# Performance work log

Measured on AMD Instinct MI355X. Metric: run time of the kernel, lower is better.

## Reference

```python
import jax, jax.numpy as jnp
import numpy as np

N = 384      # max_nodes
H = 256      # layers[0] == layers[1] == layers[2]
Z = 128      # dim_z
ED = 128     # edge_dim
AH = ED // 2 # attention hidden

# complete directed graph: combinations (i<j) then reversed pairs
_i, _j = np.triu_indices(N, k=1)
_SRC = jnp.asarray(np.concatenate([_i, _j]), dtype=jnp.int32)  # edge_index[0]
_DST = jnp.asarray(np.concatenate([_j, _i]), dtype=jnp.int32)  # edge_index[1]


def setup_inputs() -> dict:
    key = jax.random.key(0)
    ks = jax.random.split(key, 16)
    def p(k, shape, fan_in):
        return jax.random.normal(k, shape, dtype=jnp.float32) * (1.0 / np.sqrt(fan_in))
    return {
        "z": jax.random.normal(ks[0], (1, Z), dtype=jnp.float32),
        # GRU (torch layout: W_ih [3H, Z], W_hh [3H, H]; gate order r, z, n)
        "gru_Wih": p(ks[1], (3 * H, Z), Z),
        "gru_Whh": p(ks[2], (3 * H, H), H),
        "gru_bih": jnp.zeros((3 * H,), jnp.float32),
        "gru_bhh": jnp.zeros((3 * H,), jnp.float32),
        # edge_generator MLP: 2H -> 4H -> ED
        "eg_W1": p(ks[3], (2 * H, 4 * H), 2 * H), "eg_b1": jnp.zeros((4 * H,), jnp.float32),
        "eg_W2": p(ks[4], (4 * H, ED), 4 * H),   "eg_b2": jnp.zeros((ED,), jnp.float32),
        # attention MLPs: (ED+H) -> ED//2 -> 1
        "att0_W1": p(ks[5], (ED + H, AH), ED + H), "att0_b1": jnp.zeros((AH,), jnp.float32),
        "att0_W2": p(ks[6], (AH, 1), AH),           "att0_b2": jnp.zeros((1,), jnp.float32),
        "att1_W1": p(ks[7], (ED + H, AH), ED + H), "att1_b1": jnp.zeros((AH,), jnp.float32),
        "att1_W2": p(ks[8], (AH, 1), AH),           "att1_b2": jnp.zeros((1,), jnp.float32),
        # EdgeConv output linears: H -> H
        "conv0_W": p(ks[9], (H, H), H),  "conv0_b": jnp.zeros((H,), jnp.float32),
        "conv1_W": p(ks[10], (H, H), H), "conv1_b": jnp.zeros((H,), jnp.float32),
    }


def _forward(z, gru_Wih, gru_Whh, gru_bih, gru_bhh,
             eg_W1, eg_b1, eg_W2, eg_b2,
             att0_W1, att0_b1, att0_W2, att0_b2,
             att1_W1, att1_b1, att1_W2, att1_b2,
             conv0_W, conv0_b, conv1_W, conv1_b):
    # --- GRU node generation: input is the same latent z at every step ---
    gi = z[0] @ gru_Wih.T + gru_bih            # [3H], constant per step
    gir, giz, gin = jnp.split(gi, 3)
    def step(h, _):
        gh = h @ gru_Whh.T + gru_bhh
        ghr, ghz, ghn = jnp.split(gh, 3)
        r = jax.nn.sigmoid(gir + ghr)
        u = jax.nn.sigmoid(giz + ghz)
        n = jnp.tanh(gin + r * ghn)
        h2 = (1.0 - u) * n + u * h
        return h2, h2
    _, nodes = jax.lax.scan(step, jnp.zeros((H,), z.dtype), None, length=N)  # [N, H]

    # --- edge features over the complete directed graph ---
    pairs = jnp.concatenate([nodes[_SRC], nodes[_DST]], axis=-1)            # [E, 2H]
    edges = jax.nn.relu(pairs @ eg_W1 + eg_b1) @ eg_W2 + eg_b2              # [E, ED]

    # --- EdgeConv: gather src, attention MLP gate, scatter-sum, linear ---
    def conv(x, aW1, ab1, aW2, ab2, W, b):
        xs = x[_SRC]                                                        # [E, H]
        a_in = jnp.concatenate([edges, xs], axis=-1)                        # [E, ED+H]
        att = jax.nn.sigmoid(jax.nn.relu(a_in @ aW1 + ab1) @ aW2 + ab2)     # [E, 1]
        agg = jax.ops.segment_sum(att * xs, _DST, num_segments=N)           # [N, H]
        return agg @ W + b

    x = jax.nn.relu(conv(nodes, att0_W1, att0_b1, att0_W2, att0_b2, conv0_W, conv0_b))
    x = conv(x, att1_W1, att1_b1, att1_W2, att1_b2, conv1_W, conv1_b)
    return jnp.sum(x, axis=0)                                               # [H]


def reference(z, gru_Wih, gru_Whh, gru_bih, gru_bhh,
              eg_W1, eg_b1, eg_W2, eg_b2,
              att0_W1, att0_b1, att0_W2, att0_b2,
              att1_W1, att1_b1, att1_W2, att1_b2,
              conv0_W, conv0_b, conv1_W, conv1_b):
    return _forward(z, gru_Wih, gru_Whh, gru_bih, gru_bhh,
                    eg_W1, eg_b1, eg_W2, eg_b2,
                    att0_W1, att0_b1, att0_W2, att0_b2,
                    att1_W1, att1_b1, att1_W2, att1_b2,
                    conv0_W, conv0_b, conv1_W, conv1_b)
```

## Files before the change

kernel.cpp:

```cpp
#include <hip/hip_runtime.h>
#include <hip/hip_fp16.h>
#include <cstdint>

#define DEV static __device__ __forceinline__

typedef _Float16 h2v __attribute__((ext_vector_type(2)));
typedef _Float16 half8 __attribute__((ext_vector_type(8)));
typedef float float4v __attribute__((ext_vector_type(4)));

union U32H2 { uint32_t u; _Float16 f[2]; };

DEV uint32_t pack_f2(float a, float b) {
    auto p = __builtin_amdgcn_cvt_pkrtz(a, b);
    return __builtin_bit_cast(uint32_t, p);
}

DEV half8 bc8(uint4 v) { return __builtin_bit_cast(half8, v); }

DEV void gl_lds16(const void* gsrc, void* ldst) {
    __builtin_amdgcn_global_load_lds(
        (const __attribute__((address_space(1))) uint32_t*)gsrc,
        (__attribute__((address_space(3))) uint32_t*)ldst, 16, 0, 0);
}

DEV float pick4(float4v lo, float4v hi, int bsel, int r) {
    float v0 = bsel ? hi[0] : lo[0];
    float v1 = bsel ? hi[1] : lo[1];
    float v2 = bsel ? hi[2] : lo[2];
    float v3 = bsel ? hi[3] : lo[3];
    float x01 = (r & 1) ? v1 : v0;
    float x23 = (r & 1) ? v3 : v2;
    return (r & 2) ? x23 : x01;
}

static const size_t OFF_W16T  = 0;
static const size_t OFF_GI    = 98304;
static const size_t OFF_CC    = 99072;
static const size_t OFF_BF    = 99200;
static const size_t OFF_NODES = 164736;
static const size_t OFF_PF    = 263040;
static const size_t OFF_QF    = 459648;
static const size_t OFF_R0    = 656256;
static const size_t OFF_R1    = 680832;
static const size_t OFF_TT    = 705408;
static const size_t OFF_ATT0  = 10142592;
static const size_t OFF_ATT1  = 10290048;
static const size_t OFF_X0    = 10535808;
static const size_t OFF_CS    = 10634112;
static const size_t WS_TOTAL  = 10634816;

__global__ void k_prep_wl(const float* __restrict__ Whh, uint32_t* __restrict__ WL,
                          const float* __restrict__ z, const float* __restrict__ Wih,
                          const float* __restrict__ bih, const float* __restrict__ bhh,
                          float* __restrict__ gs) {
    int bb = blockIdx.x, tid = threadIdx.x;
    if (bb < 48) {
        int c = bb;
        int rt = c >> 3, kt = c & 7;
        int lane = tid & 63, wv = tid >> 6;
        int row = (rt >> 1) * 256 + wv * 32 + ((rt & 1) << 4) + (lane & 15);
        int k0 = kt*32 + (lane >> 4)*8;
        const float* src = Whh + row*256 + k0;
        uint4 o;
        o.x = pack_f2(src[0], src[1]);
        o.y = pack_f2(src[2], src[3]);
        o.z = pack_f2(src[4], src[5]);
        o.w = pack_f2(src[6], src[7]);
        ((uint4*)WL)[c*512 + tid] = o;
    } else {
        int o = (bb - 48) * 512 + tid;
        if (o < 768) {
            float acc = bih[o];
            if (o < 512) acc += bhh[o];
            for (int i = 0; i < 128; ++i) acc += Wih[o*128 + i] * z[i];
            gs[o] = acc;
        }
    }
}

__global__ void __launch_bounds__(512, 2)
k_gru_bf(const float* __restrict__ gs, const float* __restrict__ bhh,
         const uint32_t* __restrict__ WL, float* __restrict__ nodes,
         const float* __restrict__ egW2, const float* __restrict__ egb2,
         const float* __restrict__ a0W1, const float* __restrict__ a1W1,
         uint32_t* __restrict__ BF, float* __restrict__ cc) {
    int bb = blockIdx.x, tid = threadIdx.x;
    if (bb == 0) {
        __shared__ __align__(16) _Float16 hh16[512];
        int lane = tid & 63, wv = tid >> 6;
        int kq = lane >> 4, c = lane & 15;
        const float L2E = 1.44269504088896f;
        int r = c & 3, bsel = (c >> 2) & 1;
        int gidx = wv*32 + kq*4 + r + bsel*16;
        bool active = (c < 8);

        uint4 w[48];
        const uint4* wl4 = (const uint4*)WL;
        #pragma unroll
        for (int q = 0; q < 48; ++q) w[q] = wl4[q*512 + tid];
        #pragma unroll
        for (int q = 0; q < 48; ++q)
            asm volatile("" : "+a"(w[q].x), "+a"(w[q].y), "+a"(w[q].z), "+a"(w[q].w));

        float pr = -L2E * gs[gidx];
        float pz = -L2E * gs[256 + gidx];
        float pn = -2.f * L2E * gs[512 + gidx];
        float bn_l = bhh[512 + gidx];

        float h = 0.f;
        if (tid < 256) ((uint32_t*)hh16)[tid] = 0u;
        __syncthreads();

        const float4v z4 = {0.f, 0.f, 0.f, 0.f};
        int par = 0;
        for (int t = 0; t < 384; ++t) {
            const _Float16* hb = hh16 + par*256 + kq*8;
            uint4 b[8];
            #pragma unroll
            for (int kt = 0; kt < 8; ++kt) b[kt] = *(const uint4*)(hb + kt*32);

            float4v d0, d1, d2, d3, d4, d5;
            d0 = __builtin_amdgcn_mfma_f32_16x16x32_f16(bc8(w[0]),  bc8(b[0]), z4, 0, 0, 0);
            d1 = __builtin_amdgcn_mfma_f32_16x16x32_f16(bc8(w[8]),  bc8(b[0]), z4, 0, 0, 0);
            #pragma unroll
            for (int kt = 1; kt < 8; ++kt) {
                d0 = __builtin_amdgcn_mfma_f32_16x16x32_f16(bc8(w[kt]),   bc8(b[kt]), d0, 0, 0, 0);
                d1 = __builtin_amdgcn_mfma_f32_16x16x32_f16(bc8(w[8+kt]), bc8(b[kt]), d1, 0, 0, 0);
            }
            float ghr = pick4(d0, d1, bsel, r);
            float er = __builtin_amdgcn_exp2f(__builtin_fmaf(ghr, -L2E, pr));
            float rg = __builtin_amdgcn_rcpf(1.f + er);

            d2 = __builtin_amdgcn_mfma_f32_16x16x32_f16(bc8(w[16]), bc8(b[0]), z4, 0, 0, 0);
            d3 = __builtin_amdgcn_mfma_f32_16x16x32_f16(bc8(w[24]), bc8(b[0]), z4, 0, 0, 0);
            d4 = __builtin_amdgcn_mfma_f32_16x16x32_f16(bc8(w[32]), bc8(b[0]), z4, 0, 0, 0);
            d5 = __builtin_amdgcn_mfma_f32_16x16x32_f16(bc8(w[40]), bc8(b[0]), z4, 0, 0, 0);
            #pragma unroll
            for (int kt = 1; kt < 8; ++kt) {
                d2 = __builtin_amdgcn_mfma_f32_16x16x32_f16(bc8(w[16+kt]), bc8(b[kt]), d2, 0, 0, 0);
                d3 = __builtin_amdgcn_mfma_f32_16x16x32_f16(bc8(w[24+kt]), bc8(b[kt]), d3, 0, 0, 0);
                d4 = __builtin_amdgcn_mfma_f32_16x16x32_f16(bc8(w[32+kt]), bc8(b[kt]), d4, 0, 0, 0);
                d5 = __builtin_amdgcn_mfma_f32_16x16x32_f16(bc8(w[40+kt]), bc8(b[kt]), d5, 0, 0, 0);
            }

            float ghz = pick4(d2, d3, bsel, r);
            float ghn = pick4(d4, d5, bsel, r);
            float eu = __builtin_amdgcn_exp2f(__builtin_fmaf(ghz, -L2E, pz));
            float u  = __builtin_amdgcn_rcpf(1.f + eu);
            float tm = ghn + bn_l;
            float q  = __builtin_fmaf(rg * tm, -2.f * L2E, pn);
            float e2 = __builtin_amdgcn_exp2f(q);
            float nn = __builtin_fmaf(2.f, __builtin_amdgcn_rcpf(1.f + e2), -1.f);
            h = nn + u * (h - nn);

            if (active) {
                hh16[(par ^ 1)*256 + gidx] = (_Float16)h;
                nodes[t*256 + gidx] = h;
            }
            asm volatile("s_waitcnt lgkmcnt(0)" ::: "memory");
            __builtin_amdgcn_sched_barrier(0);
            __builtin_amdgcn_s_barrier();
            __builtin_amdgcn_sched_barrier(0);
            par ^= 1;
        }
    } else if (bb < 129) {
        int idx = (bb - 1) * 512 + tid;
        int k2 = idx >> 7, n = idx & 127;
        const float* A = (n < 64) ? (a0W1 + n) : (a1W1 + (n - 64));
        const float* w0 = egW2 + (2*k2) * 128;
        float a = 0.f, b = 0.f;
        for (int i = 0; i < 128; ++i) {
            float av = A[i*64];
            a += w0[i] * av;
            b += w0[128 + i] * av;
        }
        int kk = k2 >> 4, jgrp = (k2 >> 2) & 3, sub = k2 & 3;
        int lane = jgrp*16 + (n & 15), t = n >> 4;
        BF[((kk*8 + t)*64 + lane)*4 + sub] = pack_f2(a, b);
    } else {
        if (tid < 128) {
            const float* A = (tid < 64) ? a0W1 : a1W1;
            int j = tid & 63;
            float acc = 0.f;
            for (int i = 0; i < 128; ++i) acc += egb2[i] * A[i*64 + j];
            cc[tid] = acc;
        }
    }
}

__global__ void k_pq(const float* __restrict__ nodes, const float* __restrict__ eg_W1,
                     const float* __restrict__ eg_b1, const float* __restrict__ a0W1,
                     const float* __restrict__ a0b1, const float* __restrict__ cc,
                     uint32_t* __restrict__ PF, uint32_t* __restrict__ QF,
                     float* __restrict__ R0) {
    int tid = threadIdx.x;
    int s0 = blockIdx.x * 4;
    __shared__ float ns[4][256];
    #pragma unroll
    for (int q = 0; q < 4; ++q) ns[q][tid] = nodes[(s0+q)*256 + tid];
    __syncthreads();

    int k0 = tid * 4;
    float acc[4][4];
    #pragma unroll
    for (int q = 0; q < 4; ++q) { acc[q][0]=0;acc[q][1]=0;acc[q][2]=0;acc[q][3]=0; }
    for (int i = 0; i < 256; ++i) {
        float4 wv = *(const float4*)&eg_W1[i*1024 + k0];
        #pragma unroll
        for (int q = 0; q < 4; ++q) {
            float nv = ns[q][i];
            acc[q][0] += nv*wv.x; acc[q][1] += nv*wv.y;
            acc[q][2] += nv*wv.z; acc[q][3] += nv*wv.w;
        }
    }
    float4 bv = *(const float4*)&eg_b1[k0];
    {
        int kk = k0 >> 5;
        int lgrp = ((k0 >> 3) & 3) * 16;
        int sub = (k0 & 7) >> 1;
        #pragma unroll
        for (int q = 0; q < 4; ++q) {
            int s = s0 + q, g = s >> 4, srow = s & 15;
            uint2 pw;
            pw.x = pack_f2(acc[q][0] + bv.x, acc[q][1] + bv.y);
            pw.y = pack_f2(acc[q][2] + bv.z, acc[q][3] + bv.w);
            *(uint2*)(PF + (((g*32 + kk)*64 + lgrp + srow) << 2) + sub) = pw;
        }
    }

    #pragma unroll
    for (int q = 0; q < 4; ++q) { acc[q][0]=0;acc[q][1]=0;acc[q][2]=0;acc[q][3]=0; }
    for (int i = 0; i < 256; ++i) {
        float4 wv = *(const float4*)&eg_W1[(256+i)*1024 + k0];
        #pragma unroll
        for (int q = 0; q < 4; ++q) {
            float nv = ns[q][i];
            acc[q][0] += nv*wv.x; acc[q][1] += nv*wv.y;
            acc[q][2] += nv*wv.z; acc[q][3] += nv*wv.w;
        }
    }
    #pragma unroll
    for (int q = 0; q < 4; ++q) {
        uint2 pw;
        pw.x = pack_f2(acc[q][0], acc[q][1]);
        pw.y = pack_f2(acc[q][2], acc[q][3]);
        ((uint2*)QF)[(s0+q)*256 + tid] = pw;
    }

    int srow = tid >> 6, j = tid & 63;
    float racc = a0b1[j] + cc[j];
    for (int i = 0; i < 256; ++i) racc += ns[srow][i] * a0W1[(128+i)*64 + j];
    R0[(s0+srow)*64 + j] = racc;
}

__global__ void __launch_bounds__(512, 4)
k_phaseA(const uint32_t* __restrict__ PF, const uint32_t* __restrict__ QF,
         const uint32_t* __restrict__ BF, const float* __restrict__ R0,
         const float* __restrict__ a0W2, const float* __restrict__ a0b2,
         uint32_t* __restrict__ TT, float* __restrict__ ATT0) {
    __shared__ __align__(16) char smem[69632];
    uint4* Qs4 = (uint4*)smem;
    char* bufbase = smem + 32768;
    int tid = threadIdx.x;
    int lane = tid & 63, wv = tid >> 6;
    int g = blockIdx.x, dt = blockIdx.y, d0 = dt * 16;

    {
        const char* src = (const char*)(QF + (size_t)d0 * 512);
        for (int off = tid*16; off < 32768; off += 8192)
            gl_lds16(src + off, (char*)Qs4 + off);
    }
    {
        const char* psrc = (const char*)(PF + (size_t)g * 8192);
        if (tid < 128) gl_lds16(psrc + tid*16, bufbase + tid*16);
        const char* bsrc = (const char*)BF;
        #pragma unroll
        for (int i = 0; i < 2; ++i)
            gl_lds16(bsrc + tid*16 + i*8192, bufbase + 2048 + tid*16 + i*8192);
    }
    asm volatile("s_waitcnt vmcnt(0)" ::: "memory");
    __builtin_amdgcn_sched_barrier(0);
    __builtin_amdgcn_s_barrier();
    __builtin_amdgcn_sched_barrier(0);

    float4v acc[2][8];
    #pragma unroll
    for (int t = 0; t < 2; ++t)
        #pragma unroll
        for (int n = 0; n < 8; ++n) acc[t][n] = 0.f;

    for (int hc = 0; hc < 16; ++hc) {
        char* cur = bufbase + (hc & 1) * 18432;
        char* nxt = bufbase + ((hc + 1) & 1) * 18432;
        if (hc < 15) {
            const char* psrc = (const char*)(PF + ((size_t)g*32 + (size_t)(hc+1)*2) * 256);
            if (tid < 128) gl_lds16(psrc + tid*16, nxt + tid*16);
            const char* bsrc = (const char*)(BF + (size_t)(hc+1) * 4096);
            #pragma unroll
            for (int i = 0; i < 2; ++i)
                gl_lds16(bsrc + tid*16 + i*8192, nxt + 2048 + tid*16 + i*8192);
        }
        uint4* Ph = (uint4*)cur;
        uint4* Bh = (uint4*)(cur + 2048);
        #pragma unroll
        for (int kkl = 0; kkl < 2; ++kkl) {
            int kkg = hc*2 + kkl;
            half8 b[8];
            #pragma unroll
            for (int n = 0; n < 8; ++n) b[n] = bc8(Bh[(kkl*8 + n)*64 + lane]);
            half8 p8 = bc8(Ph[kkl*64 + lane]);
            #pragma unroll
            for (int t = 0; t < 2; ++t) {
                half8 q8 = bc8(Qs4[(wv*2 + t)*128 + kkg*4 + (lane >> 4)]);
                half8 x = p8 + q8;
                half8 zz = 0;
                x = __builtin_elementwise_max(x, zz);
                #pragma unroll
                for (int n = 0; n < 8; ++n)
                    acc[t][n] = __builtin_amdgcn_mfma_f32_16x16x32_f16(x, b[n], acc[t][n], 0, 0, 0);
            }
        }
        asm volatile("s_waitcnt vmcnt(0)" ::: "memory");
        __builtin_amdgcn_sched_barrier(0);
        __builtin_amdgcn_s_barrier();
        __builtin_amdgcn_sched_barrier(0);
    }

    __syncthreads();
    float* R0s = (float*)smem;
    float* w2s = (float*)(smem + 4096);
    for (int i = tid; i < 1024; i += 512)
        R0s[i] = R0[(size_t)(g*16 + (i >> 6))*64 + (i & 63)];
    if (tid < 64) w2s[tid] = a0W2[tid];
    float b2v = a0b2[0];

    _Float16* epi = (_Float16*)(smem + 32768);
    int cn = lane & 15, rhi = (lane >> 4) * 4;
    for (int half = 0; half < 2; ++half) {
        __syncthreads();
        #pragma unroll
        for (int t = 0; t < 2; ++t) {
            int dl = wv*2 + t;
            #pragma unroll
            for (int n = 0; n < 4; ++n) {
                int j = n*16 + cn;
                float4v v = acc[t][half*4 + n];
                #pragma unroll
                for (int r = 0; r < 4; ++r)
                    epi[((rhi + r)*16 + dl)*64 + j] = (_Float16)v[r];
            }
        }
        __syncthreads();
        if (half == 1) {
            int p = tid >> 1, sub = tid & 1;
            int srow = p >> 4, dl = p & 15;
            const uint4* src = (const uint4*)(epi + (size_t)p*64);
            uint4* dst = (uint4*)(TT + ((size_t)((g*16 + srow)*384 + d0 + dl))*32);
            #pragma unroll
            for (int q = 0; q < 4; ++q) dst[sub*4 + q] = src[sub*4 + q];
        }
        if (half == 0 && tid < 256) {
            int sl = tid >> 4, dl = tid & 15;
            const _Float16* tp = epi + (size_t)(sl*16 + dl)*64;
            const float* rp = R0s + sl*64;
            float logit = b2v;
            #pragma unroll
            for (int j = 0; j < 64; ++j)
                logit += fmaxf((float)tp[j] + rp[j], 0.f) * w2s[j];
            float a = 1.f / (1.f + __expf(-logit));
            int s = g*16 + sl, d = d0 + dl;
            ATT0[(size_t)s*384 + d] = (s == d) ? 0.f : a;
        }
    }
}

__global__ void k_att(const uint32_t* __restrict__ TT, const float* __restrict__ R,
                      const float* __restrict__ w2, const float* __restrict__ b2,
                      float* __restrict__ ATT, float* __restrict__ CS) {
    int tid = threadIdx.x;
    int p = blockIdx.x * 256 + tid;
    int s = p / 384, d = p - s * 384;
    int sa = (blockIdx.x * 256) / 384;
    __shared__ float w2s[64];
    __shared__ float rs[2][64];
    if (tid < 64) w2s[tid] = w2[tid];
    else if (tid < 128) rs[0][tid - 64] = R[sa*64 + (tid - 64)];
    else if (tid < 192) {
        int sb = sa + 1;
        rs[1][tid - 128] = (sb < 384) ? R[sb*64 + (tid - 128)] : 0.f;
    }
    __syncthreads();
    const uint4* tp = (const uint4*)(TT + (size_t)p*32);
    const float* rp = (s == sa) ? rs[0] : rs[1];
    float logit = b2[0];
    #pragma unroll
    for (int m = 0; m < 8; ++m) {
        uint4 tv = tp[m];
        uint32_t us[4] = {tv.x, tv.y, tv.z, tv.w};
        #pragma unroll
        for (int q = 0; q < 4; ++q) {
            U32H2 c; c.u = us[q];
            int j = m*8 + q*2;
            float h0 = fmaxf((float)c.f[0] + rp[j],   0.f);
            float h1 = fmaxf((float)c.f[1] + rp[j+1], 0.f);
            logit += h0*w2s[j] + h1*w2s[j+1];
        }
    }
    float a = 1.f / (1.f + __expf(-logit));
    float a_eff = (s == d) ? 0.f : a;
    ATT[p] = a_eff;

    float va = (s == sa) ? a_eff : 0.f;
    float vb = (s != sa) ? a_eff : 0.f;
    #pragma unroll
    for (int o = 32; o > 0; o >>= 1) {
        va += __shfl_down(va, o, 64);
        vb += __shfl_down(vb, o, 64);
    }
    if ((tid & 63) == 0) {
        atomicAdd(&CS[sa], va);
        int sb = sa + 1;
        if (sb < 384) atomicAdd(&CS[sb], vb);
    }
}

__global__ void __launch_bounds__(256)
k_aggx0(const float* __restrict__ ATT, const float* __restrict__ X,
        const float* __restrict__ W, const float* __restrict__ b,
        const float* __restrict__ a1W1, const float* __restrict__ a1b1,
        const float* __restrict__ cc,
        float* __restrict__ X0, float* __restrict__ R1, float* __restrict__ CS) {
    int d = blockIdx.x, tid = threadIdx.x;
    if (d == 0) {
        for (int s = tid; s < 384; s += 256) CS[s] = 0.f;
    }
    __shared__ float att_col[384];
    __shared__ float ag[256];
    __shared__ float xs[256];
    for (int s = tid; s < 384; s += 256) att_col[s] = ATT[(size_t)s*384 + d];
    __syncthreads();
    float acc = 0.f;
    #pragma unroll 4
    for (int s = 0; s < 384; ++s)
        acc += att_col[s] * X[(size_t)s*256 + tid];
    ag[tid] = acc;
    __syncthreads();
    float x0 = b[tid];
    for (int i = 0; i < 256; ++i) x0 += ag[i] * W[i*256 + tid];
    x0 = fmaxf(x0, 0.f);
    X0[(size_t)d*256 + tid] = x0;
    xs[tid] = x0;
    __syncthreads();
    if (tid < 64) {
        float r = a1b1[tid] + cc[64 + tid];
        for (int i = 0; i < 256; ++i) r += xs[i] * a1W1[(128+i)*64 + tid];
        R1[(size_t)d*64 + tid] = r;
    }
}

__global__ void k_vout(const float* __restrict__ CS, const float* __restrict__ X0,
                       const float* __restrict__ W, const float* __restrict__ b,
                       float* __restrict__ out) {
    int tid = threadIdx.x;
    __shared__ float cs[384];
    __shared__ float vs[256];
    for (int q = tid; q < 384; q += 256) cs[q] = CS[q];
    __syncthreads();
    float acc = 0.f;
    for (int s = 0; s < 384; s += 4) {
        acc += cs[s]*X0[s*256 + tid] + cs[s+1]*X0[(s+1)*256 + tid]
             + cs[s+2]*X0[(s+2)*256 + tid] + cs[s+3]*X0[(s+3)*256 + tid];
    }
    vs[tid] = acc;
    __syncthreads();
    float o = 384.f * b[tid];
    for (int i = 0; i < 256; ++i) o += vs[i] * W[i*256 + tid];
    out[tid] = o;
}

extern "C" void kernel_launch(void* const* d_in, const int* in_sizes, int n_in,
                              void* d_out, int out_size, void* d_ws, size_t ws_size,
                              hipStream_t stream) {
    if (ws_size < WS_TOTAL * sizeof(uint32_t)) return;

    const float* z    = (const float*)d_in[0];
    const float* Wih  = (const float*)d_in[1];
    const float* Whh  = (const float*)d_in[2];
    const float* bih  = (const float*)d_in[3];
    const float* bhh  = (const float*)d_in[4];
    const float* egW1 = (const float*)d_in[5];
    const float* egb1 = (const float*)d_in[6];
    const float* egW2 = (const float*)d_in[7];
    const float* egb2 = (const float*)d_in[8];
    const float* a0W1 = (const float*)d_in[9];
    const float* a0b1 = (const float*)d_in[10];
    const float* a0W2 = (const float*)d_in[11];
    const float* a0b2 = (const float*)d_in[12];
    const float* a1W1 = (const float*)d_in[13];
    const float* a1b1 = (const float*)d_in[14];
    const float* a1W2 = (const float*)d_in[15];
    const float* a1b2 = (const float*)d_in[16];
    const float* c0W  = (const float*)d_in[17];
    const float* c0b  = (const float*)d_in[18];
    const float* c1W  = (const float*)d_in[19];
    const float* c1b  = (const float*)d_in[20];

    uint32_t* ws   = (uint32_t*)d_ws;
    uint32_t* WL   = ws + OFF_W16T;
    float*    gs   = (float*)(ws + OFF_GI);
    float*    cc   = (float*)(ws + OFF_CC);
    uint32_t* BF   = ws + OFF_BF;
    float*    nodes= (float*)(ws + OFF_NODES);
    uint32_t* PF   = ws + OFF_PF;
    uint32_t* QF   = ws + OFF_QF;
    float*    R0   = (float*)(ws + OFF_R0);
    float*    R1   = (float*)(ws + OFF_R1);
    uint32_t* TT   = ws + OFF_TT;
    float*    ATT0 = (float*)(ws + OFF_ATT0);
    float*    ATT1 = (float*)(ws + OFF_ATT1);
    float*    X0   = (float*)(ws + OFF_X0);
    float*    CS   = (float*)(ws + OFF_CS);
    float*    out  = (float*)d_out;

    hipLaunchKernelGGL(k_prep_wl, dim3(50),     dim3(512), 0, stream, Whh, WL, z, Wih, bih, bhh, gs);
    hipLaunchKernelGGL(k_gru_bf,  dim3(130),    dim3(512), 0, stream, gs, bhh, WL, nodes,
                       egW2, egb2, a0W1, a1W1, BF, cc);
    hipLaunchKernelGGL(k_pq,      dim3(96),     dim3(256), 0, stream, nodes, egW1, egb1, a0W1, a0b1, cc, PF, QF, R0);
    hipLaunchKernelGGL(k_phaseA,  dim3(24, 24), dim3(512), 0, stream, PF, QF, BF, R0, a0W2, a0b2, TT, ATT0);
    hipLaunchKernelGGL(k_aggx0,   dim3(384),    dim3(256), 0, stream, ATT0, nodes, c0W, c0b, a1W1, a1b1, cc, X0, R1, CS);
    hipLaunchKernelGGL(k_att,     dim3(576),    dim3(256), 0, stream, TT, R1, a1W2, a1b2, ATT1, CS);
    hipLaunchKernelGGL(k_vout,    dim3(1),      dim3(256), 0, stream, CS, X0, c1W, c1b, out);
}
```

Baseline: 664.1 us.

## Split GRU recurrence across kernels to overlap node projection with tail steps

The 384-step GRU is split into two launches: the first runs steps 0-287, and the second runs steps 288-383 in block 0 while 36 other blocks compute the edge-MLP/attention projections (P, Q, R0) for the first 288 nodes. A small tail kernel then handles the remaining 96 nodes. The projection kernel is also widened to 512 threads and 8 nodes per block, with P and Q handled by separate thread halves. The unused ATT1 store in k_att is removed. The aim is to hide projection work behind the serial recurrence, at the cost of an extra launch and reloading the GRU weights into registers a second time.

After: 650.4 us, median of 2. 2.1% less time.

```diff
diff --git a/kernel.cpp b/kernel.cpp
--- a/kernel.cpp
+++ b/kernel.cpp
@@ -78,91 +78,158 @@
     }
 }
 
+DEV void gru_run(const float* __restrict__ gs, const float* __restrict__ bhh,
+                 const uint32_t* __restrict__ WL, float* __restrict__ nodes,
+                 _Float16* hh16, int tid, int t0, int t1) {
+    int lane = tid & 63, wv = tid >> 6;
+    int kq = lane >> 4, c = lane & 15;
+    const float L2E = 1.44269504088896f;
+    int r = c & 3, bsel = (c >> 2) & 1;
+    int gidx = wv*32 + kq*4 + r + bsel*16;
+    bool active = (c < 8);
+
+    uint4 w[48];
+    const uint4* wl4 = (const uint4*)WL;
+    #pragma unroll
+    for (int q = 0; q < 48; ++q) w[q] = wl4[q*512 + tid];
+    #pragma unroll
+    for (int q = 0; q < 48; ++q)
+        asm volatile("" : "+a"(w[q].x), "+a"(w[q].y), "+a"(w[q].z), "+a"(w[q].w));
+
+    float pr = -L2E * gs[gidx];
+    float pz = -L2E * gs[256 + gidx];
+    float pn = -2.f * L2E * gs[512 + gidx];
+    float bn_l = bhh[512 + gidx];
+
+    float h;
+    if (t0 == 0) {
+        h = 0.f;
+        if (tid < 256) ((uint32_t*)hh16)[tid] = 0u;
+    } else {
+        h = nodes[(size_t)(t0-1)*256 + gidx];
+        if (tid < 256) hh16[tid] = (_Float16)nodes[(size_t)(t0-1)*256 + tid];
+    }
+    __syncthreads();
+
+    const float4v z4 = {0.f, 0.f, 0.f, 0.f};
+    int par = 0;
+    for (int t = t0; t < t1; ++t) {
+        const _Float16* hb = hh16 + par*256 + kq*8;
+        uint4 b[8];
+        #pragma unroll
+        for (int kt = 0; kt < 8; ++kt) b[kt] = *(const uint4*)(hb + kt*32);
+
+        float4v d0, d1, d2, d3, d4, d5;
+        d0 = __builtin_amdgcn_mfma_f32_16x16x32_f16(bc8(w[0]),  bc8(b[0]), z4, 0, 0, 0);
+        d1 = __builtin_amdgcn_mfma_f32_16x16x32_f16(bc8(w[8]),  bc8(b[0]), z4, 0, 0, 0);
+        #pragma unroll
+        for (int kt = 1; kt < 8; ++kt) {
+            d0 = __builtin_amdgcn_mfma_f32_16x16x32_f16(bc8(w[kt]),   bc8(b[kt]), d0, 0, 0, 0);
+            d1 = __builtin_amdgcn_mfma_f32_16x16x32_f16(bc8(w[8+kt]), bc8(b[kt]), d1, 0, 0, 0);
+        }
+        float ghr = pick4(d0, d1, bsel, r);
+        float er = __builtin_amdgcn_exp2f(__builtin_fmaf(ghr, -L2E, pr));
+        float rg = __builtin_amdgcn_rcpf(1.f + er);
+
+        d2 = __builtin_amdgcn_mfma_f32_16x16x32_f16(bc8(w[16]), bc8(b[0]), z4, 0, 0, 0);
+        d3 = __builtin_amdgcn_mfma_f32_16x16x32_f16(bc8(w[24]), bc8(b[0]), z4, 0, 0, 0);
+        d4 = __builtin_amdgcn_mfma_f32_16x16x32_f16(bc8(w[32]), bc8(b[0]), z4, 0, 0, 0);
+        d5 = __builtin_amdgcn_mfma_f32_16x16x32_f16(bc8(w[40]), bc8(b[0]), z4, 0, 0, 0);
+        #pragma unroll
+        for (int kt = 1; kt < 8; ++kt) {
+            d2 = __builtin_amdgcn_mfma_f32_16x16x32_f16(bc8(w[16+kt]), bc8(b[kt]), d2, 0, 0, 0);
+            d3 = __builtin_amdgcn_mfma_f32_16x16x32_f16(bc8(w[24+kt]), bc8(b[kt]), d3, 0, 0, 0);
+            d4 = __builtin_amdgcn_mfma_f32_16x16x32_f16(bc8(w[32+kt]), bc8(b[kt]), d4, 0, 0, 0);
+            d5 = __builtin_amdgcn_mfma_f32_16x16x32_f16(bc8(w[40+kt]), bc8(b[kt]), d5, 0, 0, 0);
+        }
+
+        float ghz = pick4(d2, d3, bsel, r);
+        float ghn = pick4(d4, d5, bsel, r);
+        float eu = __builtin_amdgcn_exp2f(__builtin_fmaf(ghz, -L2E, pz));
+        float u  = __builtin_amdgcn_rcpf(1.f + eu);
+        float tm = ghn + bn_l;
+        float q  = __builtin_fmaf(rg * tm, -2.f * L2E, pn);
+        float e2 = __builtin_amdgcn_exp2f(q);
+        float nn = __builtin_fmaf(2.f, __builtin_amdgcn_rcpf(1.f + e2), -1.f);
+        h = nn + u * (h - nn);
+
+        if (active) {
+            hh16[(par ^ 1)*256 + gidx] = (_Float16)h;
+            nodes[(size_t)t*256 + gidx] = h;
+        }
+        asm volatile("s_waitcnt lgkmcnt(0)" ::: "memory");
+        __builtin_amdgcn_sched_barrier(0);
+        __builtin_amdgcn_s_barrier();
+        __builtin_amdgcn_sched_barrier(0);
+        par ^= 1;
+    }
+}
+
+DEV void pq8_body(const float* __restrict__ nodes, const float* __restrict__ egW1,
+                  const float* __restrict__ egb1, const float* __restrict__ a0W1,
+                  const float* __restrict__ a0b1, const float* __restrict__ cc,
+                  uint32_t* __restrict__ PF, uint32_t* __restrict__ QF,
+                  float* __restrict__ R0, int s0, int tid, float* ns) {
+    for (int i = tid; i < 2048; i += 512)
+        ns[i] = nodes[(size_t)s0*256 + i];
+    __syncthreads();
+
+    int tp = tid & 255;
+    int k0 = tp * 4;
+    bool isQ = tid >= 256;
+    float acc[8][4];
+    #pragma unroll
+    for (int q = 0; q < 8; ++q) { acc[q][0]=0;acc[q][1]=0;acc[q][2]=0;acc[q][3]=0; }
+    const float* Wbase = egW1 + (isQ ? (size_t)256*1024 : 0) + k0;
+    for (int i = 0; i < 256; ++i) {
+        float4 wv = *(const float4*)&Wbase[(size_t)i*1024];
+        #pragma unroll
+        for (int q = 0; q < 8; ++q) {
+            float nv = ns[q*256 + i];
+            acc[q][0] += nv*wv.x; acc[q][1] += nv*wv.y;
+            acc[q][2] += nv*wv.z; acc[q][3] += nv*wv.w;
+        }
+    }
+    if (!isQ) {
+        float4 bv = *(const float4*)&egb1[k0];
+        int kk = k0 >> 5;
+        int lgrp = ((k0 >> 3) & 3) * 16;
+        int sub = (k0 & 7) >> 1;
+        #pragma unroll
+        for (int q = 0; q < 8; ++q) {
+            int s = s0 + q, g = s >> 4, srow = s & 15;
+            uint2 pw;
+            pw.x = pack_f2(acc[q][0] + bv.x, acc[q][1] + bv.y);
+            pw.y = pack_f2(acc[q][2] + bv.z, acc[q][3] + bv.w);
+            *(uint2*)(PF + (((g*32 + kk)*64 + lgrp + srow) << 2) + sub) = pw;
+        }
+    } else {
+        #pragma unroll
+        for (int q = 0; q < 8; ++q) {
+            uint2 pw;
+            pw.x = pack_f2(acc[q][0], acc[q][1]);
+            pw.y = pack_f2(acc[q][2], acc[q][3]);
+            ((uint2*)QF)[(size_t)(s0+q)*256 + tp] = pw;
+        }
+    }
+    {
+        int srow = tid >> 6, j = tid & 63;
+        float racc = a0b1[j] + cc[j];
+        for (int i = 0; i < 256; ++i) racc += ns[srow*256 + i] * a0W1[(128+i)*64 + j];
+        R0[(size_t)(s0+srow)*64 + j] = racc;
+    }
+}
+
 __global__ void __launch_bounds__(512, 2)
-k_gru_bf(const float* __restrict__ gs, const float* __restrict__ bhh,
-         const uint32_t* __restrict__ WL, float* __restrict__ nodes,
-         const float* __restrict__ egW2, const float* __restrict__ egb2,
-         const float* __restrict__ a0W1, const float* __restrict__ a1W1,
-         uint32_t* __restrict__ BF, float* __restrict__ cc) {
+k_gruA_bf(const float* __restrict__ gs, const float* __restrict__ bhh,
+          const uint32_t* __restrict__ WL, float* __restrict__ nodes,
+          const float* __restrict__ egW2, const float* __restrict__ egb2,
+          const float* __restrict__ a0W1, const float* __restrict__ a1W1,
+          uint32_t* __restrict__ BF, float* __restrict__ cc) {
     int bb = blockIdx.x, tid = threadIdx.x;
     if (bb == 0) {
         __shared__ __align__(16) _Float16 hh16[512];
-        int lane = tid & 63, wv = tid >> 6;
-        int kq = lane >> 4, c = lane & 15;
-        const float L2E = 1.44269504088896f;
-        int r = c & 3, bsel = (c >> 2) & 1;
-        int gidx = wv*32 + kq*4 + r + bsel*16;
-        bool active = (c < 8);
-
-        uint4 w[48];
-        const uint4* wl4 = (const uint4*)WL;
-        #pragma unroll
-        for (int q = 0; q < 48; ++q) w[q] = wl4[q*512 + tid];
-        #pragma unroll
-        for (int q = 0; q < 48; ++q)
-            asm volatile("" : "+a"(w[q].x), "+a"(w[q].y), "+a"(w[q].z), "+a"(w[q].w));
-
-        float pr = -L2E * gs[gidx];
-        float pz = -L2E * gs[256 + gidx];
-        float pn = -2.f * L2E * gs[512 + gidx];
-        float bn_l = bhh[512 + gidx];
-
-        float h = 0.f;
-        if (tid < 256) ((uint32_t*)hh16)[tid] = 0u;
-        __syncthreads();
-
-        const float4v z4 = {0.f, 0.f, 0.f, 0.f};
-        int par = 0;
-        for (int t = 0; t < 384; ++t) {
-            const _Float16* hb = hh16 + par*256 + kq*8;
-            uint4 b[8];
-            #pragma unroll
-            for (int kt = 0; kt < 8; ++kt) b[kt] = *(const uint4*)(hb + kt*32);
-
-            float4v d0, d1, d2, d3, d4, d5;
-            d0 = __builtin_amdgcn_mfma_f32_16x16x32_f16(bc8(w[0]),  bc8(b[0]), z4, 0, 0, 0);
-            d1 = __builtin_amdgcn_mfma_f32_16x16x32_f16(bc8(w[8]),  bc8(b[0]), z4, 0, 0, 0);
-            #pragma unroll
-            for (int kt = 1; kt < 8; ++kt) {
-                d0 = __builtin_amdgcn_mfma_f32_16x16x32_f16(bc8(w[kt]),   bc8(b[kt]), d0, 0, 0, 0);
-                d1 = __builtin_amdgcn_mfma_f32_16x16x32_f16(bc8(w[8+kt]), bc8(b[kt]), d1, 0, 0, 0);
-            }
-            float ghr = pick4(d0, d1, bsel, r);
-            float er = __builtin_amdgcn_exp2f(__builtin_fmaf(ghr, -L2E, pr));
-            float rg = __builtin_amdgcn_rcpf(1.f + er);
-
-            d2 = __builtin_amdgcn_mfma_f32_16x16x32_f16(bc8(w[16]), bc8(b[0]), z4, 0, 0, 0);
-            d3 = __builtin_amdgcn_mfma_f32_16x16x32_f16(bc8(w[24]), bc8(b[0]), z4, 0, 0, 0);
-            d4 = __builtin_amdgcn_mfma_f32_16x16x32_f16(bc8(w[32]), bc8(b[0]), z4, 0, 0, 0);
-            d5 = __builtin_amdgcn_mfma_f32_16x16x32_f16(bc8(w[40]), bc8(b[0]), z4, 0, 0, 0);
-            #pragma unroll
-            for (int kt = 1; kt < 8; ++kt) {
-                d2 = __builtin_amdgcn_mfma_f32_16x16x32_f16(bc8(w[16+kt]), bc8(b[kt]), d2, 0, 0, 0);
-                d3 = __builtin_amdgcn_mfma_f32_16x16x32_f16(bc8(w[24+kt]), bc8(b[kt]), d3, 0, 0, 0);
-                d4 = __builtin_amdgcn_mfma_f32_16x16x32_f16(bc8(w[32+kt]), bc8(b[kt]), d4, 0, 0, 0);
-                d5 = __builtin_amdgcn_mfma_f32_16x16x32_f16(bc8(w[40+kt]), bc8(b[kt]), d5, 0, 0, 0);
-            }
-
-            float ghz = pick4(d2, d3, bsel, r);
-            float ghn = pick4(d4, d5, bsel, r);
-            float eu = __builtin_amdgcn_exp2f(__builtin_fmaf(ghz, -L2E, pz));
-            float u  = __builtin_amdgcn_rcpf(1.f + eu);
-            float tm = ghn + bn_l;
-            float q  = __builtin_fmaf(rg * tm, -2.f * L2E, pn);
-            float e2 = __builtin_amdgcn_exp2f(q);
-            float nn = __builtin_fmaf(2.f, __builtin_amdgcn_rcpf(1.f + e2), -1.f);
-            h = nn + u * (h - nn);
-
-            if (active) {
-                hh16[(par ^ 1)*256 + gidx] = (_Float16)h;
-                nodes[t*256 + gidx] = h;
-            }
-            asm volatile("s_waitcnt lgkmcnt(0)" ::: "memory");
-            __builtin_amdgcn_sched_barrier(0);
-            __builtin_amdgcn_s_barrier();
-            __builtin_amdgcn_sched_barrier(0);
-            par ^= 1;
-        }
+        gru_run(gs, bhh, WL, nodes, hh16, tid, 0, 288);
     } else if (bb < 129) {
         int idx = (bb - 1) * 512 + tid;
         int k2 = idx >> 7, n = idx & 127;
@@ -188,69 +255,32 @@
     }
 }
 
-__global__ void k_pq(const float* __restrict__ nodes, const float* __restrict__ eg_W1,
-                     const float* __restrict__ eg_b1, const float* __restrict__ a0W1,
-                     const float* __restrict__ a0b1, const float* __restrict__ cc,
-                     uint32_t* __restrict__ PF, uint32_t* __restrict__ QF,
-                     float* __restrict__ R0) {
-    int tid = threadIdx.x;
-    int s0 = blockIdx.x * 4;
-    __shared__ float ns[4][256];
-    #pragma unroll
-    for (int q = 0; q < 4; ++q) ns[q][tid] = nodes[(s0+q)*256 + tid];
-    __syncthreads();
-
-    int k0 = tid * 4;
-    float acc[4][4];
-    #pragma unroll
-    for (int q = 0; q < 4; ++q) { acc[q][0]=0;acc[q][1]=0;acc[q][2]=0;acc[q][3]=0; }
-    for (int i = 0; i < 256; ++i) {
-        float4 wv = *(const float4*)&eg_W1[i*1024 + k0];
-        #pragma unroll
-        for (int q = 0; q < 4; ++q) {
-            float nv = ns[q][i];
-            acc[q][0] += nv*wv.x; acc[q][1] += nv*wv.y;
-            acc[q][2] += nv*wv.z; acc[q][3] += nv*wv.w;
-        }
-    }
-    float4 bv = *(const float4*)&eg_b1[k0];
-    {
-        int kk = k0 >> 5;
-        int lgrp = ((k0 >> 3) & 3) * 16;
-        int sub = (k0 & 7) >> 1;
-        #pragma unroll
-        for (int q = 0; q < 4; ++q) {
-            int s = s0 + q, g = s >> 4, srow = s & 15;
-            uint2 pw;
-            pw.x = pack_f2(acc[q][0] + bv.x, acc[q][1] + bv.y);
-            pw.y = pack_f2(acc[q][2] + bv.z, acc[q][3] + bv.w);
-            *(uint2*)(PF + (((g*32 + kk)*64 + lgrp + srow) << 2) + sub) = pw;
-        }
-    }
-
-    #pragma unroll
-    for (int q = 0; q < 4; ++q) { acc[q][0]=0;acc[q][1]=0;acc[q][2]=0;acc[q][3]=0; }
-    for (int i = 0; i < 256; ++i) {
-        float4 wv = *(const float4*)&eg_W1[(256+i)*1024 + k0];
-        #pragma unroll
-        for (int q = 0; q < 4; ++q) {
-            float nv = ns[q][i];
-            acc[q][0] += nv*wv.x; acc[q][1] += nv*wv.y;
-            acc[q][2] += nv*wv.z; acc[q][3] += nv*wv.w;
-        }
-    }
-    #pragma unroll
-    for (int q = 0; q < 4; ++q) {
-        uint2 pw;
-        pw.x = pack_f2(acc[q][0], acc[q][1]);
-        pw.y = pack_f2(acc[q][2], acc[q][3]);
-        ((uint2*)QF)[(s0+q)*256 + tid] = pw;
-    }
-
-    int srow = tid >> 6, j = tid & 63;
-    float racc = a0b1[j] + cc[j];
-    for (int i = 0; i < 256; ++i) racc += ns[srow][i] * a0W1[(128+i)*64 + j];
-    R0[(s0+srow)*64 + j] = racc;
+__global__ void __launch_bounds__(512, 2)
+k_gruB_pq(const float* __restrict__ gs, const float* __restrict__ bhh,
+          const uint32_t* __restrict__ WL, float* __restrict__ nodes,
+          const float* __restrict__ egW1, const float* __restrict__ egb1,
+          const float* __restrict__ a0W1, const float* __restrict__ a0b1,
+          const float* __restrict__ cc,
+          uint32_t* __restrict__ PF, uint32_t* __restrict__ QF,
+          float* __restrict__ R0) {
+    __shared__ __align__(16) float smem_f[2048];
+    int bb = blockIdx.x, tid = threadIdx.x;
+    if (bb == 0) {
+        gru_run(gs, bhh, WL, nodes, (_Float16*)smem_f, tid, 288, 384);
+    } else {
+        pq8_body(nodes, egW1, egb1, a0W1, a0b1, cc, PF, QF, R0, (bb - 1) * 8, tid, smem_f);
+    }
+}
+
+__global__ void __launch_bounds__(512)
+k_pq_tail(const float* __restrict__ nodes, const float* __restrict__ egW1,
+          const float* __restrict__ egb1, const float* __restrict__ a0W1,
+          const float* __restrict__ a0b1, const float* __restrict__ cc,
+          uint32_t* __restrict__ PF, uint32_t* __restrict__ QF,
+          float* __restrict__ R0) {
+    __shared__ __align__(16) float smem_f[2048];
+    pq8_body(nodes, egW1, egb1, a0W1, a0b1, cc, PF, QF, R0, 288 + blockIdx.x * 8,
+             threadIdx.x, smem_f);
 }
 
 __global__ void __launch_bounds__(512, 4)
@@ -376,7 +406,7 @@
 
 __global__ void k_att(const uint32_t* __restrict__ TT, const float* __restrict__ R,
                       const float* __restrict__ w2, const float* __restrict__ b2,
-                      float* __restrict__ ATT, float* __restrict__ CS) {
+                      float* __restrict__ CS) {
     int tid = threadIdx.x;
     int p = blockIdx.x * 256 + tid;
     int s = p / 384, d = p - s * 384;
@@ -408,7 +438,6 @@
     }
     float a = 1.f / (1.f + __expf(-logit));
     float a_eff = (s == d) ? 0.f : a;
-    ATT[p] = a_eff;
 
     float va = (s == sa) ? a_eff : 0.f;
     float vb = (s != sa) ? a_eff : 0.f;
@@ -517,17 +546,19 @@
     float*    R1   = (float*)(ws + OFF_R1);
     uint32_t* TT   = ws + OFF_TT;
     float*    ATT0 = (float*)(ws + OFF_ATT0);
-    float*    ATT1 = (float*)(ws + OFF_ATT1);
     float*    X0   = (float*)(ws + OFF_X0);
     float*    CS   = (float*)(ws + OFF_CS);
     float*    out  = (float*)d_out;
 
     hipLaunchKernelGGL(k_prep_wl, dim3(50),     dim3(512), 0, stream, Whh, WL, z, Wih, bih, bhh, gs);
-    hipLaunchKernelGGL(k_gru_bf,  dim3(130),    dim3(512), 0, stream, gs, bhh, WL, nodes,
+    hipLaunchKernelGGL(k_gruA_bf, dim3(130),    dim3(512), 0, stream, gs, bhh, WL, nodes,
                        egW2, egb2, a0W1, a1W1, BF, cc);
-    hipLaunchKernelGGL(k_pq,      dim3(96),     dim3(256), 0, stream, nodes, egW1, egb1, a0W1, a0b1, cc, PF, QF, R0);
+    hipLaunchKernelGGL(k_gruB_pq, dim3(37),     dim3(512), 0, stream, gs, bhh, WL, nodes,
+                       egW1, egb1, a0W1, a0b1, cc, PF, QF, R0);
+    hipLaunchKernelGGL(k_pq_tail, dim3(12),     dim3(512), 0, stream, nodes, egW1, egb1,
+                       a0W1, a0b1, cc, PF, QF, R0);
     hipLaunchKernelGGL(k_phaseA,  dim3(24, 24), dim3(512), 0, stream, PF, QF, BF, R0, a0W2, a0b2, TT, ATT0);
     hipLaunchKernelGGL(k_aggx0,   dim3(384),    dim3(256), 0, stream, ATT0, nodes, c0W, c0b, a1W1, a1b1, cc, X0, R1, CS);
-    hipLaunchKernelGGL(k_att,     dim3(576),    dim3(256), 0, stream, TT, R1, a1W2, a1b2, ATT1, CS);
+    hipLaunchKernelGGL(k_att,     dim3(576),    dim3(256), 0, stream, TT, R1, a1W2, a1b2, CS);
     hipLaunchKernelGGL(k_vout,    dim3(1),      dim3(256), 0, stream, CS, X0, c1W, c1b, out);
 }
```
